# Optimization experiments

Measured on AMD Instinct MI355X. Metric: run time of the kernel, lower is better.

Reference implementation:

```python
import jax, jax.numpy as jnp
import numpy as np

N_NODES = 100000
K_HOPS = 2


def _add_self_loops(edge_index, n):
    loop = jnp.arange(n, dtype=edge_index.dtype)
    src = jnp.concatenate([edge_index[0], loop])
    dst = jnp.concatenate([edge_index[1], loop])
    return src, dst


def _gcn_norm(src, dst, n):
    # symmetric normalization D^-1/2 (A+I) D^-1/2
    deg = jax.ops.segment_sum(jnp.ones_like(dst, dtype=jnp.float32), dst, num_segments=n)
    dinv = jnp.where(deg > 0, jax.lax.rsqrt(deg), 0.0)
    return dinv[src] * dinv[dst]  # [E]


def setup_inputs() -> dict:
    key = jax.random.key(0)
    k1, k2, k3, k4, k5 = jax.random.split(key, 5)
    in_f, out_f = 128, 64
    x = jax.random.normal(k1, (N_NODES, in_f), dtype=jnp.float32)
    edge_index = jax.random.randint(k2, (2, 1600000), 0, N_NODES, dtype=jnp.int64)
    s1 = 1.0 / np.sqrt(in_f)
    W1 = jax.random.uniform(k3, (in_f, in_f), dtype=jnp.float32, minval=-s1, maxval=s1)
    b1 = jnp.zeros((in_f,), dtype=jnp.float32)
    W2 = jax.random.uniform(k4, (out_f, in_f), dtype=jnp.float32, minval=-s1, maxval=s1)
    b2 = jnp.zeros((out_f,), dtype=jnp.float32)
    return {"x": x, "edge_index": edge_index, "W1": W1, "b1": b1, "W2": W2, "b2": b2}


def reference(x, edge_index, W1, b1, W2, b2):
    n = x.shape[0]
    src, dst = _add_self_loops(edge_index, n)
    norm = _gcn_norm(src, dst, n)
    for _ in range(K_HOPS):
        msg = x[src] * norm[:, None]                      # [E+N, F] gather
        x = jax.ops.segment_sum(msg, dst, num_segments=n)  # scatter-add
    # transform: Linear -> ReLU -> Linear -> log_softmax
    h = jax.nn.relu(x @ W1.T + b1)
    logits = h @ W2.T + b2
    return jax.nn.log_softmax(logits, axis=1)
```

## Files before the change

### kernel.cpp

```cpp
#include <hip/hip_runtime.h>
#include <math.h>

#define CAP 64
#define NSLICE 128
#define SLMAX 784
#define QCAP 25000

typedef __attribute__((ext_vector_type(8))) short short8;
typedef __attribute__((ext_vector_type(4))) float f32x4;
typedef __attribute__((ext_vector_type(4))) int int4v;

static __device__ inline unsigned short f2bf(float f) {
    unsigned int u = __float_as_uint(f);
    u += 0x7fffu + ((u >> 16) & 1u);
    return (unsigned short)(u >> 16);
}
static __device__ inline float bf_lo(unsigned int u) { return __uint_as_float(u << 16); }
static __device__ inline float bf_hi(unsigned int u) { return __uint_as_float(u & 0xffff0000u); }
static __device__ inline unsigned int pack2(float lo, float hi) {
    return ((unsigned int)f2bf(hi) << 16) | (unsigned int)f2bf(lo);
}


__global__ __launch_bounds__(256) void part_k(
    const int* __restrict__ dst, const int* __restrict__ src, int E,
    unsigned long long mul, int2* __restrict__ queue, int* __restrict__ qcnt)
{
    __shared__ int lcnt[NSLICE];
    __shared__ int gbase[NSLICE];
    if (threadIdx.x < NSLICE) lcnt[threadIdx.x] = 0;
    __syncthreads();

    int base = blockIdx.x * 2048 + threadIdx.x * 8;
    int nv = E - base; nv = nv > 8 ? 8 : (nv < 0 ? 0 : nv);

    int d[8], sv[8], sl[8], lp[8];
    if (nv == 8) {
        int4v da = __builtin_nontemporal_load((const int4v*)(dst + base));
        int4v db = __builtin_nontemporal_load((const int4v*)(dst + base + 4));
        int4v sa = __builtin_nontemporal_load((const int4v*)(src + base));
        int4v sb = __builtin_nontemporal_load((const int4v*)(src + base + 4));
#pragma unroll
        for (int j = 0; j < 4; j++) {
            d[j] = da[j]; sv[j] = sa[j];
            d[4 + j] = db[j]; sv[4 + j] = sb[j];
        }
    } else {
        for (int j = 0; j < nv; j++) { d[j] = dst[base + j]; sv[j] = src[base + j]; }
    }

#pragma unroll
    for (int j = 0; j < 8; j++) {
        if (j < nv) {
            sl[j] = (int)(((unsigned long long)(unsigned)d[j] * mul) >> 40);
            lp[j] = atomicAdd(&lcnt[sl[j]], 1);
        }
    }
    __syncthreads();
    if (threadIdx.x < NSLICE)
        gbase[threadIdx.x] = atomicAdd(&qcnt[threadIdx.x], lcnt[threadIdx.x]);
    __syncthreads();
#pragma unroll
    for (int j = 0; j < 8; j++) {
        if (j < nv) {
            int p = gbase[sl[j]] + lp[j];
            if (p < QCAP) queue[(size_t)sl[j] * QCAP + p] = make_int2(d[j], sv[j]);
        }
    }
}


__global__ __launch_bounds__(256) void scat_lds_k(
    const int2* __restrict__ queue, const int* __restrict__ qcnt,
    int sl, int n, int* __restrict__ cnt, float* __restrict__ dinv,
    int* __restrict__ bkt)
{
    int s  = blockIdx.x;
    int lo = s * sl;
    int hi = lo + sl < n ? lo + sl : n;
    int nn = hi - lo;
    if (nn <= 0) return;

    __shared__ int cur[SLMAX];
    for (int i = threadIdx.x; i < nn; i += 256) cur[i] = 0;
    __syncthreads();

    int m = qcnt[s]; if (m > QCAP) m = QCAP;
    const long long* __restrict__ q = (const long long*)(queue + (size_t)s * QCAP);
    for (int i = threadIdx.x; i < m; i += 256) {
        long long r = __builtin_nontemporal_load(q + i);
        int d  = (int)(r & 0xffffffffll);
        int sv = (int)(r >> 32);
        int pos = atomicAdd(&cur[d - lo], 1);
        if (pos < CAP) bkt[(size_t)d * CAP + pos] = sv;
    }
    __syncthreads();
    for (int i = threadIdx.x; i < nn; i += 256) {
        int c = cur[i];
        cnt[lo + i] = c;
        dinv[lo + i] = rsqrtf((float)(c + 1));
    }
}


__global__ void conv_x_k(const float2* __restrict__ x, const float* __restrict__ dinv,
                         unsigned int* __restrict__ xb, int n) {
    int i = blockIdx.x * blockDim.x + threadIdx.x;
    if (i < n * 64) {
        float sc = dinv[i >> 6];
        float2 v = x[i];
        xb[i] = pack2(v.x * sc, v.y * sc);
    }
}

__global__ void conv_w2_k(const float2* __restrict__ w1, unsigned int* __restrict__ o1, int n1,
                          const float2* __restrict__ w2, unsigned int* __restrict__ o2, int n2) {
    int i = blockIdx.x * blockDim.x + threadIdx.x;
    if (i < n1) {
        float2 v = w1[i];
        o1[i] = pack2(v.x, v.y);
    } else if (i < n1 + n2) {
        float2 v = w2[i - n1];
        o2[i - n1] = pack2(v.x, v.y);
    }
}


template<bool SQ>
__global__ __launch_bounds__(256) void gather_b_k(
    const unsigned int* __restrict__ xin,
    const int* __restrict__ cnt, const int* __restrict__ bkt,
    const float* __restrict__ dinv,
    unsigned int* __restrict__ xout, int n)
{
    int v = blockIdx.x * 4 + (threadIdx.x >> 6);
    if (v >= n) return;
    int l = threadIdx.x & 63;
    int c = cnt[v]; if (c > CAP) c = CAP;

    int be = bkt[(size_t)v * CAP + l];
    unsigned int us = xin[(size_t)v * 64 + l];
    float ax = 0.f, ay = 0.f;

    int i = 0;
    for (; i + 8 <= c; i += 8) {
        unsigned int u[8];
#pragma unroll
        for (int j = 0; j < 8; j++) {
            int s = __builtin_amdgcn_readlane(be, i + j);
            u[j] = xin[(size_t)s * 64 + l];
        }
#pragma unroll
        for (int j = 0; j < 8; j++) { ax += bf_lo(u[j]); ay += bf_hi(u[j]); }
    }
    for (; i + 4 <= c; i += 4) {
        unsigned int u[4];
#pragma unroll
        for (int j = 0; j < 4; j++) {
            int s = __builtin_amdgcn_readlane(be, i + j);
            u[j] = xin[(size_t)s * 64 + l];
        }
#pragma unroll
        for (int j = 0; j < 4; j++) { ax += bf_lo(u[j]); ay += bf_hi(u[j]); }
    }
    for (; i < c; i++) {
        int s = __builtin_amdgcn_readlane(be, i);
        unsigned int u = xin[(size_t)s * 64 + l];
        ax += bf_lo(u); ay += bf_hi(u);
    }

    ax += bf_lo(us);
    ay += bf_hi(us);

    float dv = dinv[v];
    float sc = SQ ? dv * dv : dv;
    xout[(size_t)v * 64 + l] = pack2(ax * sc, ay * sc);
}

__global__ __launch_bounds__(256) void transform_mfma_k(
    const unsigned short* __restrict__ x2b,
    const unsigned short* __restrict__ w1b,
    const float* __restrict__ b1,
    const unsigned short* __restrict__ w2b,
    const float* __restrict__ b2,
    float* __restrict__ out, int n)
{
    __shared__ __align__(16) unsigned short Hs[64][152];

    int t = threadIdx.x;
    int w = t >> 6;
    int l = t & 63;
    int lg = l >> 4;
    int ll = l & 15;
    int node0 = blockIdx.x * 64;

    int nrow = node0 + w * 16 + ll;
    int crow = nrow < n ? nrow : (n - 1);
    const unsigned short* xrow = x2b + (size_t)crow * 128 + lg * 8;
    short8 a[4];
#pragma unroll
    for (int kb = 0; kb < 4; kb++)
        a[kb] = *(const short8*)(xrow + kb * 32);

    f32x4 acc[8];
#pragma unroll
    for (int nt = 0; nt < 8; nt++) {
        float bv = b1[nt * 16 + ll];
        acc[nt][0] = bv; acc[nt][1] = bv; acc[nt][2] = bv; acc[nt][3] = bv;
    }
#pragma unroll
    for (int nt = 0; nt < 8; nt++) {
        const unsigned short* wrow = w1b + (size_t)(nt * 16 + ll) * 128 + lg * 8;
#pragma unroll
        for (int kb = 0; kb < 4; kb++) {
            short8 bf = *(const short8*)(wrow + kb * 32);
            acc[nt] = __builtin_amdgcn_mfma_f32_16x16x32_bf16(a[kb], bf, acc[nt], 0, 0, 0);
        }
    }

#pragma unroll
    for (int nt = 0; nt < 8; nt++) {
#pragma unroll
        for (int r = 0; r < 4; r++) {
            float hv = fmaxf(acc[nt][r], 0.f);
            Hs[w * 16 + lg * 4 + r][nt * 16 + ll] = f2bf(hv);
        }
    }

    short8 ha[4];
#pragma unroll
    for (int kb = 0; kb < 4; kb++)
        ha[kb] = *(const short8*)&Hs[w * 16 + ll][kb * 32 + lg * 8];

    f32x4 acc2[4];
#pragma unroll
    for (int nt = 0; nt < 4; nt++) {
        float bv = b2[nt * 16 + ll];
        acc2[nt][0] = bv; acc2[nt][1] = bv; acc2[nt][2] = bv; acc2[nt][3] = bv;
        const unsigned short* wrow = w2b + (size_t)(nt * 16 + ll) * 128 + lg * 8;
#pragma unroll
        for (int kb = 0; kb < 4; kb++) {
            short8 bf = *(const short8*)(wrow + kb * 32);
            acc2[nt] = __builtin_amdgcn_mfma_f32_16x16x32_bf16(ha[kb], bf, acc2[nt], 0, 0, 0);
        }
    }

#pragma unroll
    for (int r = 0; r < 4; r++) {
        float m = fmaxf(fmaxf(acc2[0][r], acc2[1][r]), fmaxf(acc2[2][r], acc2[3][r]));
        m = fmaxf(m, __shfl_xor(m, 1));
        m = fmaxf(m, __shfl_xor(m, 2));
        m = fmaxf(m, __shfl_xor(m, 4));
        m = fmaxf(m, __shfl_xor(m, 8));
        float s = __expf(acc2[0][r] - m) + __expf(acc2[1][r] - m) +
                  __expf(acc2[2][r] - m) + __expf(acc2[3][r] - m);
        s += __shfl_xor(s, 1);
        s += __shfl_xor(s, 2);
        s += __shfl_xor(s, 4);
        s += __shfl_xor(s, 8);
        float lse = m + __logf(s);
        int node = node0 + w * 16 + lg * 4 + r;
        if (node < n) {
#pragma unroll
            for (int nt = 0; nt < 4; nt++)
                out[(size_t)node * 64 + nt * 16 + ll] = acc2[nt][r] - lse;
        }
    }
}


static inline size_t align256(size_t x) { return (x + 255) & ~(size_t)255; }

extern "C" void kernel_launch(void* const* d_in, const int* in_sizes, int n_in,
                              void* d_out, int out_size, void* d_ws, size_t ws_size,
                              hipStream_t stream) {
    const float* x  = (const float*)d_in[0];
    const int*   ei = (const int*)d_in[1];
    const float* W1 = (const float*)d_in[2];
    const float* b1 = (const float*)d_in[3];
    const float* W2 = (const float*)d_in[4];
    const float* b2 = (const float*)d_in[5];
    float* out = (float*)d_out;

    int n = in_sizes[0] / 128;
    int E = in_sizes[1] / 2;
    const int* src = ei;
    const int* dst = ei + E;

    char* w = (char*)d_ws;
    size_t off = 0;
    int*          cnt  = (int*)(w + off);          off += align256((size_t)n * sizeof(int));
    int*          qcnt = (int*)(w + off);          off += align256(NSLICE * sizeof(int));
    float*        dinv = (float*)(w + off);        off += align256((size_t)n * sizeof(float));
    int*          bkt  = (int*)(w + off);          off += align256((size_t)n * CAP * sizeof(int));
    unsigned int* xb   = (unsigned int*)(w + off); off += align256((size_t)n * 64 * sizeof(unsigned int));
    unsigned int* z1b  = (unsigned int*)(w + off); off += align256((size_t)n * 64 * sizeof(unsigned int));
    unsigned int* x2b  = (unsigned int*)(w + off); off += align256((size_t)n * 64 * sizeof(unsigned int));
    unsigned int* w1b  = (unsigned int*)(w + off); off += align256((size_t)128 * 64 * sizeof(unsigned int));
    unsigned int* w2b  = (unsigned int*)(w + off);
    int2* queue = (int2*)xb;

    int tb = 256;
    int gb_x = (n * 64 + tb - 1) / tb;
    int gb_g = (n + 3) / 4;
    int gb_p = (E + 2047) / 2048;

    int sl = (n + NSLICE - 1) / NSLICE;
    unsigned long long mul = ((1ULL << 40) + (unsigned long long)sl - 1) / (unsigned long long)sl;

    (void)hipMemsetAsync(qcnt, 0, NSLICE * sizeof(int), stream);
    part_k<<<gb_p, tb, 0, stream>>>(dst, src, E, mul, queue, qcnt);
    scat_lds_k<<<NSLICE, tb, 0, stream>>>(queue, qcnt, sl, n, cnt, dinv, bkt);

    conv_x_k<<<gb_x, tb, 0, stream>>>((const float2*)x, dinv, xb, n);
    int n1 = 128 * 64, n2 = 64 * 64;
    conv_w2_k<<<(n1 + n2 + tb - 1) / tb, tb, 0, stream>>>(
        (const float2*)W1, w1b, n1, (const float2*)W2, w2b, n2);

    gather_b_k<true ><<<gb_g, tb, 0, stream>>>(xb,  cnt, bkt, dinv, z1b, n);
    gather_b_k<false><<<gb_g, tb, 0, stream>>>(z1b, cnt, bkt, dinv, x2b, n);

    transform_mfma_k<<<(n + 63) / 64, 256, 0, stream>>>(
        (const unsigned short*)x2b, (const unsigned short*)w1b, b1,
        (const unsigned short*)w2b, b2, out, n);
}
```

Measured before the change: 242.1 us.

## Fuse x conversion, weight conversion and second hop into neighboring kernels

Folds the bf16 scaling of x into the scatter kernel. It reuses the queue buffer in place: each slice's queue region lines up exactly with its nodes' output rows. Weight conversion is merged into the partition kernel as extra blocks. The second gather hop is fused into the MFMA transform through LDS, which removes the x2b intermediate and three launches. It also doubles the slice count, sizes the queue capacity from the slice size, and adds a 16-wide unrolled gather loop. In exchange, each wave in the fused transform gathers 16 nodes one after another, and the in-place aliasing depends on the layout coincidence holding.

Result: slower. 250.0 us (+3.3%).

```diff
diff --git a/kernel.cpp b/kernel.cpp
--- a/kernel.cpp
+++ b/kernel.cpp
@@ -2,9 +2,8 @@
 #include <math.h>
 
 #define CAP 64
-#define NSLICE 128
-#define SLMAX 784
-#define QCAP 25000
+#define NSLICE 256
+#define SLMAX 392
 
 typedef __attribute__((ext_vector_type(8))) short short8;
 typedef __attribute__((ext_vector_type(4))) float f32x4;
@@ -24,11 +23,26 @@
 
 __global__ __launch_bounds__(256) void part_k(
     const int* __restrict__ dst, const int* __restrict__ src, int E,
-    unsigned long long mul, int2* __restrict__ queue, int* __restrict__ qcnt)
+    unsigned long long mul, int qcap, int2* __restrict__ queue, int* __restrict__ qcnt,
+    int gb_p,
+    const float2* __restrict__ W1f, unsigned int* __restrict__ w1b, int n1,
+    const float2* __restrict__ W2f, unsigned int* __restrict__ w2b, int n2)
 {
+    if (blockIdx.x >= gb_p) {
+        int i = (blockIdx.x - gb_p) * 256 + threadIdx.x;
+        if (i < n1) {
+            float2 v = W1f[i];
+            w1b[i] = pack2(v.x, v.y);
+        } else if (i < n1 + n2) {
+            float2 v = W2f[i - n1];
+            w2b[i - n1] = pack2(v.x, v.y);
+        }
+        return;
+    }
+
     __shared__ int lcnt[NSLICE];
     __shared__ int gbase[NSLICE];
-    if (threadIdx.x < NSLICE) lcnt[threadIdx.x] = 0;
+    lcnt[threadIdx.x] = 0;
     __syncthreads();
 
     int base = blockIdx.x * 2048 + threadIdx.x * 8;
@@ -57,23 +71,23 @@
         }
     }
     __syncthreads();
-    if (threadIdx.x < NSLICE)
-        gbase[threadIdx.x] = atomicAdd(&qcnt[threadIdx.x], lcnt[threadIdx.x]);
+    gbase[threadIdx.x] = atomicAdd(&qcnt[threadIdx.x], lcnt[threadIdx.x]);
     __syncthreads();
 #pragma unroll
     for (int j = 0; j < 8; j++) {
         if (j < nv) {
             int p = gbase[sl[j]] + lp[j];
-            if (p < QCAP) queue[(size_t)sl[j] * QCAP + p] = make_int2(d[j], sv[j]);
+            if (p < qcap) queue[(size_t)sl[j] * qcap + p] = make_int2(d[j], sv[j]);
         }
     }
 }
 
 
 __global__ __launch_bounds__(256) void scat_lds_k(
-    const int2* __restrict__ queue, const int* __restrict__ qcnt,
-    int sl, int n, int* __restrict__ cnt, float* __restrict__ dinv,
-    int* __restrict__ bkt)
+    const int2* __restrict__ queue, const int* __restrict__ qcnt, int qcap,
+    int sl, int n, const float4* __restrict__ x4,
+    int* __restrict__ cnt, float* __restrict__ dinv,
+    int* __restrict__ bkt, unsigned int* __restrict__ xb)
 {
     int s  = blockIdx.x;
     int lo = s * sl;
@@ -82,11 +96,12 @@
     if (nn <= 0) return;
 
     __shared__ int cur[SLMAX];
+    __shared__ float sdv[SLMAX];
     for (int i = threadIdx.x; i < nn; i += 256) cur[i] = 0;
     __syncthreads();
 
-    int m = qcnt[s]; if (m > QCAP) m = QCAP;
-    const long long* __restrict__ q = (const long long*)(queue + (size_t)s * QCAP);
+    int m = qcnt[s]; if (m > qcap) m = qcap;
+    const long long* __restrict__ q = (const long long*)(queue + (size_t)s * qcap);
     for (int i = threadIdx.x; i < m; i += 256) {
         long long r = __builtin_nontemporal_load(q + i);
         int d  = (int)(r & 0xffffffffll);
@@ -98,35 +113,23 @@
     for (int i = threadIdx.x; i < nn; i += 256) {
         int c = cur[i];
         cnt[lo + i] = c;
-        dinv[lo + i] = rsqrtf((float)(c + 1));
-    }
-}
-
-
-__global__ void conv_x_k(const float2* __restrict__ x, const float* __restrict__ dinv,
-                         unsigned int* __restrict__ xb, int n) {
-    int i = blockIdx.x * blockDim.x + threadIdx.x;
-    if (i < n * 64) {
-        float sc = dinv[i >> 6];
-        float2 v = x[i];
-        xb[i] = pack2(v.x * sc, v.y * sc);
-    }
-}
-
-__global__ void conv_w2_k(const float2* __restrict__ w1, unsigned int* __restrict__ o1, int n1,
-                          const float2* __restrict__ w2, unsigned int* __restrict__ o2, int n2) {
-    int i = blockIdx.x * blockDim.x + threadIdx.x;
-    if (i < n1) {
-        float2 v = w1[i];
-        o1[i] = pack2(v.x, v.y);
-    } else if (i < n1 + n2) {
-        float2 v = w2[i - n1];
-        o2[i - n1] = pack2(v.x, v.y);
-    }
-}
-
-
-template<bool SQ>
+        float dv = rsqrtf((float)(c + 1));
+        dinv[lo + i] = dv;
+        sdv[i] = dv;
+    }
+    __syncthreads();
+    for (int j = threadIdx.x; j < nn * 32; j += 256) {
+        int nl = j >> 5, f4 = j & 31;
+        float4 v = x4[(size_t)(lo + nl) * 32 + f4];
+        float sc = sdv[nl];
+        uint2 o;
+        o.x = pack2(v.x * sc, v.y * sc);
+        o.y = pack2(v.z * sc, v.w * sc);
+        ((uint2*)xb)[(size_t)(lo + nl) * 32 + f4] = o;
+    }
+}
+
+
 __global__ __launch_bounds__(256) void gather_b_k(
     const unsigned int* __restrict__ xin,
     const int* __restrict__ cnt, const int* __restrict__ bkt,
@@ -137,12 +140,23 @@
     if (v >= n) return;
     int l = threadIdx.x & 63;
     int c = cnt[v]; if (c > CAP) c = CAP;
+    c = __builtin_amdgcn_readfirstlane(c);
 
     int be = bkt[(size_t)v * CAP + l];
     unsigned int us = xin[(size_t)v * 64 + l];
     float ax = 0.f, ay = 0.f;
 
     int i = 0;
+    for (; i + 16 <= c; i += 16) {
+        unsigned int u[16];
+#pragma unroll
+        for (int j = 0; j < 16; j++) {
+            int s = __builtin_amdgcn_readlane(be, i + j);
+            u[j] = xin[(size_t)s * 64 + l];
+        }
+#pragma unroll
+        for (int j = 0; j < 16; j++) { ax += bf_lo(u[j]); ay += bf_hi(u[j]); }
+    }
     for (; i + 8 <= c; i += 8) {
         unsigned int u[8];
 #pragma unroll
@@ -173,19 +187,22 @@
     ay += bf_hi(us);
 
     float dv = dinv[v];
-    float sc = SQ ? dv * dv : dv;
+    float sc = dv * dv;
     xout[(size_t)v * 64 + l] = pack2(ax * sc, ay * sc);
 }
 
-__global__ __launch_bounds__(256) void transform_mfma_k(
-    const unsigned short* __restrict__ x2b,
-    const unsigned short* __restrict__ w1b,
-    const float* __restrict__ b1,
-    const unsigned short* __restrict__ w2b,
-    const float* __restrict__ b2,
+
+__global__ __launch_bounds__(256) void gather_transform_k(
+    const unsigned int* __restrict__ z1b,
+    const int* __restrict__ cnt, const int* __restrict__ bkt,
+    const float* __restrict__ dinv,
+    const unsigned short* __restrict__ w1b, const float* __restrict__ b1,
+    const unsigned short* __restrict__ w2b, const float* __restrict__ b2,
     float* __restrict__ out, int n)
 {
-    __shared__ __align__(16) unsigned short Hs[64][152];
+    __shared__ __align__(16) unsigned char ldsU[64 * 304];
+    unsigned int   (*X2s)[68]  = (unsigned int(*)[68])ldsU;
+    unsigned short (*Hs)[152]  = (unsigned short(*)[152])ldsU;
 
     int t = threadIdx.x;
     int w = t >> 6;
@@ -194,13 +211,41 @@
     int ll = l & 15;
     int node0 = blockIdx.x * 64;
 
-    int nrow = node0 + w * 16 + ll;
-    int crow = nrow < n ? nrow : (n - 1);
-    const unsigned short* xrow = x2b + (size_t)crow * 128 + lg * 8;
+    for (int k = 0; k < 16; k++) {
+        int vl = w * 16 + k;
+        int v = node0 + vl;
+        if (v >= n) break;
+        int c = cnt[v]; if (c > CAP) c = CAP;
+        c = __builtin_amdgcn_readfirstlane(c);
+        int be = bkt[(size_t)v * CAP + l];
+        unsigned int us = z1b[(size_t)v * 64 + l];
+        float ax = 0.f, ay = 0.f;
+        int i = 0;
+        for (; i + 8 <= c; i += 8) {
+            unsigned int u[8];
+#pragma unroll
+            for (int j = 0; j < 8; j++) {
+                int s = __builtin_amdgcn_readlane(be, i + j);
+                u[j] = z1b[(size_t)s * 64 + l];
+            }
+#pragma unroll
+            for (int j = 0; j < 8; j++) { ax += bf_lo(u[j]); ay += bf_hi(u[j]); }
+        }
+        for (; i < c; i++) {
+            int s = __builtin_amdgcn_readlane(be, i);
+            unsigned int u = z1b[(size_t)s * 64 + l];
+            ax += bf_lo(u); ay += bf_hi(u);
+        }
+        float dv = dinv[v];
+        X2s[vl][l] = pack2((ax + bf_lo(us)) * dv, (ay + bf_hi(us)) * dv);
+    }
+    __syncthreads();
+
     short8 a[4];
 #pragma unroll
     for (int kb = 0; kb < 4; kb++)
-        a[kb] = *(const short8*)(xrow + kb * 32);
+        a[kb] = *(const short8*)&X2s[w * 16 + ll][kb * 16 + lg * 4];
+    __syncthreads();
 
     f32x4 acc[8];
 #pragma unroll
@@ -287,40 +332,37 @@
     const int* src = ei;
     const int* dst = ei + E;
 
+    int sl = (n + NSLICE - 1) / NSLICE;
+    int qcap = sl * 32;
+    unsigned long long mul = ((1ULL << 40) + (unsigned long long)sl - 1) / (unsigned long long)sl;
+
     char* w = (char*)d_ws;
     size_t off = 0;
     int*          cnt  = (int*)(w + off);          off += align256((size_t)n * sizeof(int));
     int*          qcnt = (int*)(w + off);          off += align256(NSLICE * sizeof(int));
     float*        dinv = (float*)(w + off);        off += align256((size_t)n * sizeof(float));
     int*          bkt  = (int*)(w + off);          off += align256((size_t)n * CAP * sizeof(int));
-    unsigned int* xb   = (unsigned int*)(w + off); off += align256((size_t)n * 64 * sizeof(unsigned int));
+    size_t xb_bytes = (size_t)NSLICE * qcap * 8;
+    unsigned int* xb   = (unsigned int*)(w + off); off += align256(xb_bytes);
     unsigned int* z1b  = (unsigned int*)(w + off); off += align256((size_t)n * 64 * sizeof(unsigned int));
-    unsigned int* x2b  = (unsigned int*)(w + off); off += align256((size_t)n * 64 * sizeof(unsigned int));
     unsigned int* w1b  = (unsigned int*)(w + off); off += align256((size_t)128 * 64 * sizeof(unsigned int));
     unsigned int* w2b  = (unsigned int*)(w + off);
     int2* queue = (int2*)xb;
 
     int tb = 256;
-    int gb_x = (n * 64 + tb - 1) / tb;
     int gb_g = (n + 3) / 4;
     int gb_p = (E + 2047) / 2048;
-
-    int sl = (n + NSLICE - 1) / NSLICE;
-    unsigned long long mul = ((1ULL << 40) + (unsigned long long)sl - 1) / (unsigned long long)sl;
+    int n1 = 128 * 128 / 2, n2 = 64 * 128 / 2;
+    int gb_w = (n1 + n2 + tb - 1) / tb;
 
     (void)hipMemsetAsync(qcnt, 0, NSLICE * sizeof(int), stream);
-    part_k<<<gb_p, tb, 0, stream>>>(dst, src, E, mul, queue, qcnt);
-    scat_lds_k<<<NSLICE, tb, 0, stream>>>(queue, qcnt, sl, n, cnt, dinv, bkt);
-
-    conv_x_k<<<gb_x, tb, 0, stream>>>((const float2*)x, dinv, xb, n);
-    int n1 = 128 * 64, n2 = 64 * 64;
-    conv_w2_k<<<(n1 + n2 + tb - 1) / tb, tb, 0, stream>>>(
-        (const float2*)W1, w1b, n1, (const float2*)W2, w2b, n2);
-
-    gather_b_k<true ><<<gb_g, tb, 0, stream>>>(xb,  cnt, bkt, dinv, z1b, n);
-    gather_b_k<false><<<gb_g, tb, 0, stream>>>(z1b, cnt, bkt, dinv, x2b, n);
-
-    transform_mfma_k<<<(n + 63) / 64, 256, 0, stream>>>(
-        (const unsigned short*)x2b, (const unsigned short*)w1b, b1,
-        (const unsigned short*)w2b, b2, out, n);
-}
+    part_k<<<gb_p + gb_w, tb, 0, stream>>>(dst, src, E, mul, qcap, queue, qcnt,
+                                           gb_p, (const float2*)W1, w1b, n1,
+                                           (const float2*)W2, w2b, n2);
+    scat_lds_k<<<NSLICE, tb, 0, stream>>>(queue, qcnt, qcap, sl, n, (const float4*)x,
+                                          cnt, dinv, bkt, xb);
+    gather_b_k<<<gb_g, tb, 0, stream>>>(xb, cnt, bkt, dinv, z1b, n);
+    gather_transform_k<<<(n + 63) / 64, tb, 0, stream>>>(
+        z1b, cnt, bkt, dinv,
+        (const unsigned short*)w1b, b1, (const unsigned short*)w2b, b2, out, n);
+}
```
